# Kernel optimization log

Hardware: AMD Instinct MI355X
Metric: run time of the kernel (lower is better)

Reference implementation:

```python
import jax, jax.numpy as jnp
import numpy as np

B, S, H, F, E, K = 4, 2048, 1024, 4096, 8, 2

def setup_inputs() -> dict:
    key = jax.random.key(0)
    ks = jax.random.split(key, 8)
    sH = 1.0 / np.sqrt(H)
    sF = 1.0 / np.sqrt(F)
    return {
        'x':  jax.random.normal(ks[0], (B, S, H), dtype=jnp.float32),
        'W1': jax.random.uniform(ks[1], (E, H, F), jnp.float32, -sH, sH),
        'b1': jax.random.uniform(ks[2], (E, F), jnp.float32, -sH, sH),
        'W2': jax.random.uniform(ks[3], (E, F, H), jnp.float32, -sF, sF),
        'b2': jax.random.uniform(ks[4], (E, H), jnp.float32, -sF, sF),
        'Wr': jax.random.uniform(ks[5], (H, E), jnp.float32, -sH, sH),
        'br': jax.random.uniform(ks[6], (E,), jnp.float32, -sH, sH),
    }

def reference(x, W1, b1, W2, b2, Wr, br):
    # Router
    logits = jnp.einsum('bsh,he->bse', x, Wr) + br          # (B,S,E)
    probs_all = jax.nn.softmax(logits, axis=-1)
    importance = probs_all.sum(axis=(0, 1))                  # (E,)
    total_tokens = jnp.float32(B * S)
    aux_loss = E * jnp.sum((importance / total_tokens) ** 2)
    # Eval mode: no noise. Top-k gating over logits.
    topk_vals, topk_idx = jax.lax.top_k(logits, K)           # (B,S,K)
    topk_w = jax.nn.softmax(topk_vals, axis=-1)              # (B,S,K)
    # Dense all-expert FFN: Linear -> exact GELU -> Linear
    h = jnp.einsum('bsh,ehf->bsef', x, W1) + b1[None, None]  # (B,S,E,F)
    h = jax.nn.gelu(h, approximate=False)
    expert_stack = jnp.einsum('bsef,efh->bseh', h, W2) + b2[None, None]  # (B,S,E,H)
    # Scatter top-k weights into dense gating (B,S,E)
    gating = jnp.sum(jax.nn.one_hot(topk_idx, E, dtype=x.dtype) * topk_w[..., None], axis=-2)
    out = jnp.einsum('bse,bseh->bsh', gating, expert_stack)
    return out, aux_loss
```

## Files before the change

kernel.cpp:

```cpp
#include <hip/hip_runtime.h>
#include <hip/hip_bf16.h>
#include <stdint.h>

#define TOK 8192
#define HD  1024
#define FD  4096
#define NE  8
#define BK  32

#define WS_CNT 0
#define WS_RW  1024
#define WS_LST 131072
#define WS_PRB 524288
#define WS_PART 786432
#define WS_XB  ((size_t)1  << 20)
#define WS_W1T ((size_t)18 << 20)
#define WS_W2T ((size_t)84 << 20)
#define WS_H   ((size_t)150 << 20)
#define WS_Y   WS_W1T

typedef __attribute__((ext_vector_type(4))) float  f32x4;
typedef __attribute__((ext_vector_type(8))) short  s16x8;
typedef __attribute__((ext_vector_type(4))) short  s16x4;
typedef __attribute__((ext_vector_type(8))) __bf16 bf16x8;

__device__ inline unsigned short f2bf(float f) {
    __hip_bfloat16 h = __float2bfloat16(f);
    return __builtin_bit_cast(unsigned short, h);
}
__device__ inline float bf2f(unsigned short s) {
    unsigned u = ((unsigned)s) << 16;
    return __builtin_bit_cast(float, u);
}
__device__ inline f32x4 mfma_bf16(s16x8 a, s16x8 b, f32x4 c) {
    return __builtin_amdgcn_mfma_f32_16x16x32_bf16(
        __builtin_bit_cast(bf16x8, a), __builtin_bit_cast(bf16x8, b), c, 0, 0, 0);
}
__device__ inline void gl2lds16(const void* g, void* l) {
    __builtin_amdgcn_global_load_lds(
        (const __attribute__((address_space(1))) unsigned int*)g,
        (__attribute__((address_space(3))) unsigned int*)l, 16, 0, 0);
}

__global__ __launch_bounds__(256) void transpose_cvt2_kernel(
    const float* __restrict__ W1, unsigned short* __restrict__ w1t,
    const float* __restrict__ W2, unsigned short* __restrict__ w2t)
{
    __shared__ unsigned short tile[64][65];
    int id = blockIdx.x;
    int p  = blockIdx.y;
    const float* src; unsigned short* dst; int R, C, r0, c0;
    if (id < 1024) {
        src = W1; dst = w1t; R = HD; C = FD;
        c0 = (id & 63) * 64; r0 = (id >> 6) * 64;
    } else {
        int j = id - 1024;
        src = W2; dst = w2t; R = FD; C = HD;
        c0 = (j & 15) * 64; r0 = (j >> 4) * 64;
    }
    const float* s = src + ((size_t)p * R + r0) * C + c0;
    int c4   = (threadIdx.x & 15) * 4;
    int rgrp = threadIdx.x >> 4;
    #pragma unroll
    for (int i = 0; i < 4; ++i) {
        int r = i * 16 + rgrp;
        f32x4 v = *(const f32x4*)&s[(size_t)r * C + c4];
        tile[r][c4 + 0] = f2bf(v[0]); tile[r][c4 + 1] = f2bf(v[1]);
        tile[r][c4 + 2] = f2bf(v[2]); tile[r][c4 + 3] = f2bf(v[3]);
    }
    __syncthreads();
    unsigned short* d = dst + ((size_t)p * C + c0) * R + r0;
    int hq = (threadIdx.x & 15) * 4;
    int fb = threadIdx.x >> 4;
    #pragma unroll
    for (int i = 0; i < 4; ++i) {
        int c = i * 16 + fb;
        s16x4 v;
        v[0] = (short)tile[hq + 0][c]; v[1] = (short)tile[hq + 1][c];
        v[2] = (short)tile[hq + 2][c]; v[3] = (short)tile[hq + 3][c];
        *(s16x4*)&d[(size_t)c * R + hq] = v;
    }
}

__global__ __launch_bounds__(256) void router_kernel(
    const float* __restrict__ x, const float* __restrict__ Wr,
    const float* __restrict__ br, int* __restrict__ cnt,
    int* __restrict__ lists, float* __restrict__ rw,
    float* __restrict__ probs, unsigned short* __restrict__ xb)
{
    int gid  = blockIdx.x * 256 + threadIdx.x;
    int tok  = gid >> 6;
    int lane = threadIdx.x & 63;
    const float* xr = x + (size_t)tok * HD;
    unsigned short* xbr = xb + (size_t)tok * HD;
    float acc[NE] = {0.f,0.f,0.f,0.f,0.f,0.f,0.f,0.f};
    #pragma unroll
    for (int i = 0; i < 4; ++i) {
        int h0 = i * 256 + lane * 4;
        f32x4 xv = *(const f32x4*)&xr[h0];
        s16x4 xo;
        xo[0] = (short)f2bf(xv[0]); xo[1] = (short)f2bf(xv[1]);
        xo[2] = (short)f2bf(xv[2]); xo[3] = (short)f2bf(xv[3]);
        *(s16x4*)&xbr[h0] = xo;
        #pragma unroll
        for (int j = 0; j < 4; ++j) {
            const f32x4* w = (const f32x4*)(Wr + (size_t)(h0 + j) * NE);
            f32x4 w0 = w[0], w1 = w[1];
            float xs = xv[j];
            acc[0] += xs * w0[0]; acc[1] += xs * w0[1];
            acc[2] += xs * w0[2]; acc[3] += xs * w0[3];
            acc[4] += xs * w1[0]; acc[5] += xs * w1[1];
            acc[6] += xs * w1[2]; acc[7] += xs * w1[3];
        }
    }
    #pragma unroll
    for (int e = 0; e < NE; ++e) {
        float v = acc[e];
        #pragma unroll
        for (int off = 32; off > 0; off >>= 1) v += __shfl_down(v, off);
        acc[e] = v;
    }
    if (lane == 0) {
        float lg[NE];
        #pragma unroll
        for (int e = 0; e < NE; ++e) lg[e] = acc[e] + br[e];
        float m = lg[0];
        #pragma unroll
        for (int e = 1; e < NE; ++e) m = fmaxf(m, lg[e]);
        float s = 0.f, p[NE];
        #pragma unroll
        for (int e = 0; e < NE; ++e) { p[e] = __expf(lg[e] - m); s += p[e]; }
        float inv = 1.f / s;
        f32x4 p0 = {p[0]*inv, p[1]*inv, p[2]*inv, p[3]*inv};
        f32x4 p1 = {p[4]*inv, p[5]*inv, p[6]*inv, p[7]*inv};
        *(f32x4*)&probs[(size_t)tok * NE]     = p0;
        *(f32x4*)&probs[(size_t)tok * NE + 4] = p1;
        int e0 = 0;
        #pragma unroll
        for (int e = 1; e < NE; ++e) if (lg[e] > lg[e0]) e0 = e;
        int e1 = (e0 == 0) ? 1 : 0;
        #pragma unroll
        for (int e = 0; e < NE; ++e) if (e != e0 && lg[e] > lg[e1]) e1 = e;
        float t1 = __expf(lg[e1] - lg[e0]);
        float w0 = 1.f / (1.f + t1);
        rw[tok * 2 + 0] = w0;
        rw[tok * 2 + 1] = t1 * w0;
        int p0i = atomicAdd(&cnt[e0], 1);
        lists[e0 * TOK + p0i] = (tok << 1);
        int p1i = atomicAdd(&cnt[e1], 1);
        lists[e1 * TOK + p1i] = (tok << 1) | 1;
    }
}


#define GEMM_FIND_EXPERT()                                                     \
    int pb = blockIdx.y;                                                       \
    int e = 0, row0 = -1, nc = 0, base = 0;                                    \
    {                                                                          \
        int accb = 0, pref = 0;                                                \
        _Pragma("unroll")                                                      \
        for (int i = 0; i < NE; ++i) {                                         \
            int c = cnt[i];                                                    \
            int nb = (c + 127) >> 7;                                           \
            if (row0 < 0 && pb < accb + nb) {                                  \
                e = i; row0 = (pb - accb) << 7; nc = c; base = pref;           \
            }                                                                  \
            accb += nb; pref += c;                                             \
        }                                                                      \
        if (row0 < 0) return;                                                  \
    }

#define GEMM_STAGE(kt3, b3)                                                    \
    {                                                                          \
        gl2lds16(ga[0] + (size_t)(kt3) * BK, &As[b3][(w * 64) * 8]);           \
        gl2lds16(ga[1] + (size_t)(kt3) * BK, &As[b3][(256 + w * 64) * 8]);     \
        gl2lds16(gb[0] + (size_t)(kt3) * BK, &Bs[b3][(w * 64) * 8]);           \
        gl2lds16(gb[1] + (size_t)(kt3) * BK, &Bs[b3][(256 + w * 64) * 8]);     \
    }

#define GEMM_COMPUTE(b)                                                        \
    {                                                                          \
        s16x8 af[4], bfr[4];                                                   \
        _Pragma("unroll")                                                      \
        for (int mi = 0; mi < 4; ++mi) {                                       \
            int r = wr * 64 + mi * 16 + rl;                                    \
            af[mi] = *(const s16x8*)&As[b][r * 32 + ((q ^ ((r >> 1) & 3)) << 3)]; \
        }                                                                      \
        _Pragma("unroll")                                                      \
        for (int ni = 0; ni < 4; ++ni) {                                       \
            int n = wc * 64 + ni * 16 + rl;                                    \
            bfr[ni] = *(const s16x8*)&Bs[b][n * 32 + ((q ^ ((n >> 1) & 3)) << 3)]; \
        }                                                                      \
        _Pragma("unroll")                                                      \
        for (int mi = 0; mi < 4; ++mi)                                         \
            _Pragma("unroll")                                                  \
            for (int ni = 0; ni < 4; ++ni)                                     \
                acc[mi][ni] = mfma_bf16(af[mi], bfr[ni], acc[mi][ni]);         \
    }

#define GEMM_MAINLOOP(NT)                                                      \
    GEMM_STAGE(0, 0); GEMM_STAGE(1, 1);                                        \
    int bc = 0;                                                                \
    for (int kt = 0; kt < (NT); ++kt) {                                        \
        if (kt + 1 < (NT)) asm volatile("s_waitcnt vmcnt(4)" ::: "memory");    \
        else               asm volatile("s_waitcnt vmcnt(0)" ::: "memory");    \
        __builtin_amdgcn_s_barrier();                                          \
        if (kt + 2 < (NT)) {                                                   \
            int b2 = bc + 2; if (b2 >= 3) b2 -= 3;                             \
            GEMM_STAGE(kt + 2, b2);                                            \
        }                                                                      \
        GEMM_COMPUTE(bc);                                                      \
        ++bc; if (bc >= 3) bc = 0;                                             \
    }

__global__ __launch_bounds__(256, 3) void gemm1_kernel(
    const unsigned short* __restrict__ xb, const unsigned short* __restrict__ w1t,
    const float* __restrict__ b1, const int* __restrict__ cnt,
    const int* __restrict__ lists, unsigned short* __restrict__ hbuf)
{
    GEMM_FIND_EXPERT()
    int cb = blockIdx.x * 128;

    __shared__ unsigned short As[3][128 * BK];
    __shared__ unsigned short Bs[3][128 * BK];

    int tid  = threadIdx.x;
    int lane = tid & 63;
    int w    = tid >> 6;
    int wr   = w >> 1;
    int wc   = w & 1;
    int rl   = lane & 15;
    int q    = lane >> 4;

    const unsigned short* ga[2];
    const unsigned short* gb[2];
    #pragma unroll
    for (int i = 0; i < 2; ++i) {
        int ch  = i * 256 + tid;
        int row = ch >> 2;
        int kc  = (ch & 3) ^ ((row >> 1) & 3);
        int lr  = row0 + row;
        int tok = (lr < nc) ? (lists[e * TOK + lr] >> 1) : 0;
        ga[i] = xb + (size_t)tok * HD + kc * 8;
        gb[i] = w1t + ((size_t)e * FD + cb + row) * HD + kc * 8;
    }

    f32x4 acc[4][4];
    #pragma unroll
    for (int i = 0; i < 4; ++i)
        #pragma unroll
        for (int j = 0; j < 4; ++j) acc[i][j] = (f32x4){0.f, 0.f, 0.f, 0.f};

    GEMM_MAINLOOP(HD / BK)

    int col0 = cb + wc * 64 + rl;
    float b1v[4];
    #pragma unroll
    for (int ni = 0; ni < 4; ++ni) b1v[ni] = b1[e * FD + col0 + ni * 16];
    #pragma unroll
    for (int mi = 0; mi < 4; ++mi) {
        #pragma unroll
        for (int j = 0; j < 4; ++j) {
            int grow = row0 + wr * 64 + mi * 16 + q * 4 + j;
            if (grow < nc) {
                unsigned short* dst = hbuf + (size_t)(base + grow) * FD + col0;
                #pragma unroll
                for (int ni = 0; ni < 4; ++ni) {
                    float u = acc[mi][ni][j] + b1v[ni];
                    float z = 0.79788456080286536f * (u + 0.044715f * u * u * u);
                    float t = __expf(-2.f * fabsf(z));
                    float th = __fdividef(1.f - t, 1.f + t);
                    th = (z < 0.f) ? -th : th;
                    dst[ni * 16] = f2bf(0.5f * u * (1.f + th));
                }
            }
        }
    }
}

__global__ __launch_bounds__(256, 3) void gemm2_kernel(
    const unsigned short* __restrict__ hbuf, const unsigned short* __restrict__ w2t,
    const float* __restrict__ b2, const int* __restrict__ cnt,
    const int* __restrict__ lists, unsigned short* __restrict__ ybuf)
{
    GEMM_FIND_EXPERT()
    int cb = blockIdx.x * 128;

    __shared__ unsigned short As[3][128 * BK];
    __shared__ unsigned short Bs[3][128 * BK];

    int tid  = threadIdx.x;
    int lane = tid & 63;
    int w    = tid >> 6;
    int wr   = w >> 1;
    int wc   = w & 1;
    int rl   = lane & 15;
    int q    = lane >> 4;

    const unsigned short* ga[2];
    const unsigned short* gb[2];
    #pragma unroll
    for (int i = 0; i < 2; ++i) {
        int ch  = i * 256 + tid;
        int row = ch >> 2;
        int kc  = (ch & 3) ^ ((row >> 1) & 3);
        int lr  = row0 + row;
        int hrow = base + ((lr < nc) ? lr : (nc - 1));
        ga[i] = hbuf + (size_t)hrow * FD + kc * 8;
        gb[i] = w2t + ((size_t)e * HD + cb + row) * FD + kc * 8;
    }

    f32x4 acc[4][4];
    #pragma unroll
    for (int i = 0; i < 4; ++i)
        #pragma unroll
        for (int j = 0; j < 4; ++j) acc[i][j] = (f32x4){0.f, 0.f, 0.f, 0.f};

    GEMM_MAINLOOP(FD / BK)

    int col0 = cb + wc * 64 + rl;
    float b2v[4];
    #pragma unroll
    for (int ni = 0; ni < 4; ++ni) b2v[ni] = b2[e * HD + col0 + ni * 16];
    #pragma unroll
    for (int mi = 0; mi < 4; ++mi) {
        #pragma unroll
        for (int j = 0; j < 4; ++j) {
            int grow = row0 + wr * 64 + mi * 16 + q * 4 + j;
            if (grow < nc) {
                int entry = lists[e * TOK + grow];
                unsigned short* dst = ybuf + ((size_t)((entry & 1) * TOK + (entry >> 1))) * HD + col0;
                #pragma unroll
                for (int ni = 0; ni < 4; ++ni)
                    dst[ni * 16] = f2bf(acc[mi][ni][j] + b2v[ni]);
            }
        }
    }
}

__global__ __launch_bounds__(256) void gather_aux_kernel(
    const unsigned short* __restrict__ ybuf, const float* __restrict__ rw,
    float* __restrict__ out, const float* __restrict__ probs,
    float* __restrict__ partial)
{
    if (blockIdx.x < 4096) {
        int g = blockIdx.x * 256 + threadIdx.x;
        int t = g >> 7;
        int h0 = (g & 127) * 8;
        float w0 = rw[t * 2 + 0];
        float w1 = rw[t * 2 + 1];
        s16x8 y0 = *(const s16x8*)&ybuf[(size_t)t * HD + h0];
        s16x8 y1 = *(const s16x8*)&ybuf[((size_t)TOK + t) * HD + h0];
        f32x4 o0, o1;
        #pragma unroll
        for (int j = 0; j < 4; ++j) {
            o0[j] = w0 * bf2f((unsigned short)y0[j])   + w1 * bf2f((unsigned short)y1[j]);
            o1[j] = w0 * bf2f((unsigned short)y0[j+4]) + w1 * bf2f((unsigned short)y1[j+4]);
        }
        *(f32x4*)&out[(size_t)t * HD + h0]     = o0;
        *(f32x4*)&out[(size_t)t * HD + h0 + 4] = o1;
    } else {
        __shared__ float sm[256 * NE];
        int bb  = blockIdx.x - 4096;
        int tid = threadIdx.x;
        int t = bb * 256 + tid;
        const f32x4* p = (const f32x4*)&probs[(size_t)t * NE];
        f32x4 a = p[0], b = p[1];
        sm[tid*NE+0]=a[0]; sm[tid*NE+1]=a[1]; sm[tid*NE+2]=a[2]; sm[tid*NE+3]=a[3];
        sm[tid*NE+4]=b[0]; sm[tid*NE+5]=b[1]; sm[tid*NE+6]=b[2]; sm[tid*NE+7]=b[3];
        __syncthreads();
        for (int s = 128; s > 0; s >>= 1) {
            if (tid < s) {
                #pragma unroll
                for (int e2 = 0; e2 < NE; ++e2)
                    sm[tid * NE + e2] += sm[(tid + s) * NE + e2];
            }
            __syncthreads();
        }
        if (tid < NE) partial[bb * NE + tid] = sm[tid];
    }
}

__global__ __launch_bounds__(64) void aux2_kernel(
    const float* __restrict__ partial, float* __restrict__ outAux)
{
    __shared__ float sm[NE];
    int tid = threadIdx.x;
    if (tid < NE) {
        float s = 0.f;
        for (int b = 0; b < 32; ++b) s += partial[b * NE + tid];
        sm[tid] = s;
    }
    __syncthreads();
    if (tid == 0) {
        float ssum = 0.f;
        #pragma unroll
        for (int e2 = 0; e2 < NE; ++e2) {
            float v = sm[e2] * (1.f / (float)TOK);
            ssum += v * v;
        }
        outAux[0] = (float)NE * ssum;
    }
}

extern "C" void kernel_launch(void* const* d_in, const int* in_sizes, int n_in,
                              void* d_out, int out_size, void* d_ws, size_t ws_size,
                              hipStream_t stream) {
    const float* x  = (const float*)d_in[0];
    const float* W1 = (const float*)d_in[1];
    const float* b1 = (const float*)d_in[2];
    const float* W2 = (const float*)d_in[3];
    const float* b2 = (const float*)d_in[4];
    const float* Wr = (const float*)d_in[5];
    const float* br = (const float*)d_in[6];
    float* out = (float*)d_out;
    char* ws = (char*)d_ws;

    int*   cnt   = (int*)(ws + WS_CNT);
    float* rw    = (float*)(ws + WS_RW);
    int*   lists = (int*)(ws + WS_LST);
    float* probs = (float*)(ws + WS_PRB);
    float* part  = (float*)(ws + WS_PART);
    unsigned short* xb   = (unsigned short*)(ws + WS_XB);
    unsigned short* w1t  = (unsigned short*)(ws + WS_W1T);
    unsigned short* w2t  = (unsigned short*)(ws + WS_W2T);
    unsigned short* hbuf = (unsigned short*)(ws + WS_H);
    unsigned short* ybuf = (unsigned short*)(ws + WS_Y);

    hipMemsetAsync(ws, 0, 64, stream);
    router_kernel<<<TOK / 4, 256, 0, stream>>>(x, Wr, br, cnt, lists, rw, probs, xb);
    transpose_cvt2_kernel<<<dim3(2048, NE), 256, 0, stream>>>(W1, w1t, W2, w2t);
    gemm1_kernel<<<dim3(FD / 128, 136), 256, 0, stream>>>(xb, w1t, b1, cnt, lists, hbuf);
    gemm2_kernel<<<dim3(HD / 128, 136), 256, 0, stream>>>(hbuf, w2t, b2, cnt, lists, ybuf);
    gather_aux_kernel<<<4096 + 32, 256, 0, stream>>>(ybuf, rw, out, probs, part);
    aux2_kernel<<<1, 64, 0, stream>>>(part, out + (size_t)TOK * HD);
}
```

Measured before the change: 732.8 us.

## Enlarge grouped GEMM M tile to 192 rows with double-buffered LDS pipeline

The routed expert GEMMs now use 192x128 output tiles instead of 128x128. Each wave computes a 96x64 sub-tile with 24 accumulators, so more MFMA work is done per weight tile loaded and fewer blocks fit the token blocks per expert. The LDS pipeline drops from triple buffering with prefetch distance 2 to double buffering with prefetch distance 1 and two barriers per k-step. This raises register pressure and waste in partial tiles, and it may expose more memory latency from the shallower prefetch.

```diff
diff --git a/kernel.cpp b/kernel.cpp
--- a/kernel.cpp
+++ b/kernel.cpp
@@ -161,9 +161,9 @@
         _Pragma("unroll")                                                      \
         for (int i = 0; i < NE; ++i) {                                         \
             int c = cnt[i];                                                    \
-            int nb = (c + 127) >> 7;                                           \
+            int nb = (c + 191) / 192;                                          \
             if (row0 < 0 && pb < accb + nb) {                                  \
-                e = i; row0 = (pb - accb) << 7; nc = c; base = pref;           \
+                e = i; row0 = (pb - accb) * 192; nc = c; base = pref;          \
             }                                                                  \
             accb += nb; pref += c;                                             \
         }                                                                      \
@@ -174,43 +174,47 @@
     {                                                                          \
         gl2lds16(ga[0] + (size_t)(kt3) * BK, &As[b3][(w * 64) * 8]);           \
         gl2lds16(ga[1] + (size_t)(kt3) * BK, &As[b3][(256 + w * 64) * 8]);     \
+        gl2lds16(ga[2] + (size_t)(kt3) * BK, &As[b3][(512 + w * 64) * 8]);     \
         gl2lds16(gb[0] + (size_t)(kt3) * BK, &Bs[b3][(w * 64) * 8]);           \
         gl2lds16(gb[1] + (size_t)(kt3) * BK, &Bs[b3][(256 + w * 64) * 8]);     \
     }
 
 #define GEMM_COMPUTE(b)                                                        \
     {                                                                          \
-        s16x8 af[4], bfr[4];                                                   \
-        _Pragma("unroll")                                                      \
-        for (int mi = 0; mi < 4; ++mi) {                                       \
-            int r = wr * 64 + mi * 16 + rl;                                    \
-            af[mi] = *(const s16x8*)&As[b][r * 32 + ((q ^ ((r >> 1) & 3)) << 3)]; \
-        }                                                                      \
+        s16x8 bfr[4];                                                          \
         _Pragma("unroll")                                                      \
         for (int ni = 0; ni < 4; ++ni) {                                       \
             int n = wc * 64 + ni * 16 + rl;                                    \
             bfr[ni] = *(const s16x8*)&Bs[b][n * 32 + ((q ^ ((n >> 1) & 3)) << 3)]; \
         }                                                                      \
         _Pragma("unroll")                                                      \
-        for (int mi = 0; mi < 4; ++mi)                                         \
+        for (int mh = 0; mh < 2; ++mh) {                                       \
+            s16x8 af[3];                                                       \
             _Pragma("unroll")                                                  \
-            for (int ni = 0; ni < 4; ++ni)                                     \
-                acc[mi][ni] = mfma_bf16(af[mi], bfr[ni], acc[mi][ni]);         \
+            for (int mi = 0; mi < 3; ++mi) {                                   \
+                int r = wr * 96 + mh * 48 + mi * 16 + rl;                      \
+                af[mi] = *(const s16x8*)&As[b][r * 32 + ((q ^ ((r >> 1) & 3)) << 3)]; \
+            }                                                                  \
+            _Pragma("unroll")                                                  \
+            for (int mi = 0; mi < 3; ++mi)                                     \
+                _Pragma("unroll")                                              \
+                for (int ni = 0; ni < 4; ++ni)                                 \
+                    acc[mh * 3 + mi][ni] = mfma_bf16(af[mi], bfr[ni], acc[mh * 3 + mi][ni]); \
+        }                                                                      \
     }
 
 #define GEMM_MAINLOOP(NT)                                                      \
-    GEMM_STAGE(0, 0); GEMM_STAGE(1, 1);                                        \
-    int bc = 0;                                                                \
+    GEMM_STAGE(0, 0);                                                          \
     for (int kt = 0; kt < (NT); ++kt) {                                        \
-        if (kt + 1 < (NT)) asm volatile("s_waitcnt vmcnt(4)" ::: "memory");    \
-        else               asm volatile("s_waitcnt vmcnt(0)" ::: "memory");    \
         __builtin_amdgcn_s_barrier();                                          \
-        if (kt + 2 < (NT)) {                                                   \
-            int b2 = bc + 2; if (b2 >= 3) b2 -= 3;                             \
-            GEMM_STAGE(kt + 2, b2);                                            \
+        if (kt + 1 < (NT)) {                                                   \
+            GEMM_STAGE(kt + 1, (kt + 1) & 1);                                  \
+            asm volatile("s_waitcnt vmcnt(5)" ::: "memory");                   \
+        } else {                                                               \
+            asm volatile("s_waitcnt vmcnt(0)" ::: "memory");                   \
         }                                                                      \
-        GEMM_COMPUTE(bc);                                                      \
-        ++bc; if (bc >= 3) bc = 0;                                             \
+        __builtin_amdgcn_s_barrier();                                          \
+        GEMM_COMPUTE(kt & 1);                                                  \
     }
 
 __global__ __launch_bounds__(256, 3) void gemm1_kernel(
@@ -221,8 +225,8 @@
     GEMM_FIND_EXPERT()
     int cb = blockIdx.x * 128;
 
-    __shared__ unsigned short As[3][128 * BK];
-    __shared__ unsigned short Bs[3][128 * BK];
+    __shared__ unsigned short As[2][192 * BK];
+    __shared__ unsigned short Bs[2][128 * BK];
 
     int tid  = threadIdx.x;
     int lane = tid & 63;
@@ -232,22 +236,28 @@
     int rl   = lane & 15;
     int q    = lane >> 4;
 
-    const unsigned short* ga[2];
+    const unsigned short* ga[3];
     const unsigned short* gb[2];
     #pragma unroll
-    for (int i = 0; i < 2; ++i) {
+    for (int i = 0; i < 3; ++i) {
         int ch  = i * 256 + tid;
         int row = ch >> 2;
         int kc  = (ch & 3) ^ ((row >> 1) & 3);
         int lr  = row0 + row;
         int tok = (lr < nc) ? (lists[e * TOK + lr] >> 1) : 0;
         ga[i] = xb + (size_t)tok * HD + kc * 8;
+    }
+    #pragma unroll
+    for (int i = 0; i < 2; ++i) {
+        int ch  = i * 256 + tid;
+        int row = ch >> 2;
+        int kc  = (ch & 3) ^ ((row >> 1) & 3);
         gb[i] = w1t + ((size_t)e * FD + cb + row) * HD + kc * 8;
     }
 
-    f32x4 acc[4][4];
-    #pragma unroll
-    for (int i = 0; i < 4; ++i)
+    f32x4 acc[6][4];
+    #pragma unroll
+    for (int i = 0; i < 6; ++i)
         #pragma unroll
         for (int j = 0; j < 4; ++j) acc[i][j] = (f32x4){0.f, 0.f, 0.f, 0.f};
 
@@ -258,15 +268,15 @@
     #pragma unroll
     for (int ni = 0; ni < 4; ++ni) b1v[ni] = b1[e * FD + col0 + ni * 16];
     #pragma unroll
-    for (int mi = 0; mi < 4; ++mi) {
+    for (int a = 0; a < 6; ++a) {
         #pragma unroll
         for (int j = 0; j < 4; ++j) {
-            int grow = row0 + wr * 64 + mi * 16 + q * 4 + j;
+            int grow = row0 + wr * 96 + a * 16 + q * 4 + j;
             if (grow < nc) {
                 unsigned short* dst = hbuf + (size_t)(base + grow) * FD + col0;
                 #pragma unroll
                 for (int ni = 0; ni < 4; ++ni) {
-                    float u = acc[mi][ni][j] + b1v[ni];
+                    float u = acc[a][ni][j] + b1v[ni];
                     float z = 0.79788456080286536f * (u + 0.044715f * u * u * u);
                     float t = __expf(-2.f * fabsf(z));
                     float th = __fdividef(1.f - t, 1.f + t);
@@ -286,8 +296,8 @@
     GEMM_FIND_EXPERT()
     int cb = blockIdx.x * 128;
 
-    __shared__ unsigned short As[3][128 * BK];
-    __shared__ unsigned short Bs[3][128 * BK];
+    __shared__ unsigned short As[2][192 * BK];
+    __shared__ unsigned short Bs[2][128 * BK];
 
     int tid  = threadIdx.x;
     int lane = tid & 63;
@@ -297,22 +307,28 @@
     int rl   = lane & 15;
     int q    = lane >> 4;
 
-    const unsigned short* ga[2];
+    const unsigned short* ga[3];
     const unsigned short* gb[2];
     #pragma unroll
-    for (int i = 0; i < 2; ++i) {
+    for (int i = 0; i < 3; ++i) {
         int ch  = i * 256 + tid;
         int row = ch >> 2;
         int kc  = (ch & 3) ^ ((row >> 1) & 3);
         int lr  = row0 + row;
         int hrow = base + ((lr < nc) ? lr : (nc - 1));
         ga[i] = hbuf + (size_t)hrow * FD + kc * 8;
+    }
+    #pragma unroll
+    for (int i = 0; i < 2; ++i) {
+        int ch  = i * 256 + tid;
+        int row = ch >> 2;
+        int kc  = (ch & 3) ^ ((row >> 1) & 3);
         gb[i] = w2t + ((size_t)e * HD + cb + row) * FD + kc * 8;
     }
 
-    f32x4 acc[4][4];
-    #pragma unroll
-    for (int i = 0; i < 4; ++i)
+    f32x4 acc[6][4];
+    #pragma unroll
+    for (int i = 0; i < 6; ++i)
         #pragma unroll
         for (int j = 0; j < 4; ++j) acc[i][j] = (f32x4){0.f, 0.f, 0.f, 0.f};
 
@@ -323,16 +339,16 @@
     #pragma unroll
     for (int ni = 0; ni < 4; ++ni) b2v[ni] = b2[e * HD + col0 + ni * 16];
     #pragma unroll
-    for (int mi = 0; mi < 4; ++mi) {
+    for (int a = 0; a < 6; ++a) {
         #pragma unroll
         for (int j = 0; j < 4; ++j) {
-            int grow = row0 + wr * 64 + mi * 16 + q * 4 + j;
+            int grow = row0 + wr * 96 + a * 16 + q * 4 + j;
             if (grow < nc) {
                 int entry = lists[e * TOK + grow];
                 unsigned short* dst = ybuf + ((size_t)((entry & 1) * TOK + (entry >> 1))) * HD + col0;
                 #pragma unroll
                 for (int ni = 0; ni < 4; ++ni)
-                    dst[ni * 16] = f2bf(acc[mi][ni][j] + b2v[ni]);
+                    dst[ni * 16] = f2bf(acc[a][ni][j] + b2v[ni]);
             }
         }
     }
@@ -430,8 +446,8 @@
     hipMemsetAsync(ws, 0, 64, stream);
     router_kernel<<<TOK / 4, 256, 0, stream>>>(x, Wr, br, cnt, lists, rw, probs, xb);
     transpose_cvt2_kernel<<<dim3(2048, NE), 256, 0, stream>>>(W1, w1t, W2, w2t);
-    gemm1_kernel<<<dim3(FD / 128, 136), 256, 0, stream>>>(xb, w1t, b1, cnt, lists, hbuf);
-    gemm2_kernel<<<dim3(HD / 128, 136), 256, 0, stream>>>(hbuf, w2t, b2, cnt, lists, ybuf);
+    gemm1_kernel<<<dim3(FD / 128, 94), 256, 0, stream>>>(xb, w1t, b1, cnt, lists, hbuf);
+    gemm2_kernel<<<dim3(HD / 128, 94), 256, 0, stream>>>(hbuf, w2t, b2, cnt, lists, ybuf);
     gather_aux_kernel<<<4096 + 32, 256, 0, stream>>>(ybuf, rw, out, probs, part);
     aux2_kernel<<<1, 64, 0, stream>>>(part, out + (size_t)TOK * HD);
 }
```

After: 703.6 us. -4.0%, faster.
